# Kernel tuning notes

Measured on AMD Instinct MI355X. Metric: run time of the kernel, lower is better.

Reference implementation:

```python
import jax, jax.numpy as jnp
import numpy as np

B, S, D, H = 2, 2048, 4096, 32
HD = D // H
FF = 22016 // 2  # QWenMLP gets intermediate_size // 2 = 11008
EPS = 1e-6
THETA = 10000.0


def setup_inputs() -> dict:
    key = jax.random.key(0)
    ks = jax.random.split(key, 10)
    s = lambda fan_in: 1.0 / np.sqrt(fan_in)
    return {
        "positions": jnp.broadcast_to(jnp.arange(S, dtype=jnp.int32), (B, S)),
        "hidden_states": jax.random.normal(ks[0], (B, S, D), jnp.float32),
        "ln1_w": jnp.ones((D,), jnp.float32),
        "ln2_w": jnp.ones((D,), jnp.float32),
        "Wqkv": jax.random.normal(ks[1], (D, 3 * D), jnp.float32) * s(D),
        "bqkv": jax.random.normal(ks[2], (3 * D,), jnp.float32) * 0.02,
        "Wo": jax.random.normal(ks[3], (D, D), jnp.float32) * s(D),
        "W1": jax.random.normal(ks[4], (D, FF), jnp.float32) * s(D),
        "W2": jax.random.normal(ks[5], (D, FF), jnp.float32) * s(D),
        "Wout": jax.random.normal(ks[6], (FF, D), jnp.float32) * s(FF),
    }


def _rmsnorm(x, w, eps=EPS):
    return x * jax.lax.rsqrt(jnp.mean(x * x, axis=-1, keepdims=True) + eps) * w


def _rope(x, positions):
    # x: [B, S, H, HD]; NeoX-style rotate-half RoPE over full head_dim
    inv_freq = 1.0 / (THETA ** (jnp.arange(0, HD, 2, dtype=jnp.float32) / HD))
    freqs = positions.astype(jnp.float32)[..., None] * inv_freq  # [B, S, HD/2]
    cos = jnp.concatenate([jnp.cos(freqs)] * 2, axis=-1)[:, :, None, :]
    sin = jnp.concatenate([jnp.sin(freqs)] * 2, axis=-1)[:, :, None, :]
    x1, x2 = jnp.split(x, 2, axis=-1)
    rotated = jnp.concatenate([-x2, x1], axis=-1)
    return x * cos + rotated * sin


def reference(positions, hidden_states, ln1_w, ln2_w, Wqkv, bqkv, Wo, W1, W2, Wout):
    residual = hidden_states
    h = _rmsnorm(hidden_states, ln1_w)
    qkv = h @ Wqkv + bqkv                              # [B, S, 3D]
    q, k, v = jnp.split(qkv, 3, axis=-1)
    q = _rope(q.reshape(B, S, H, HD), positions)
    k = _rope(k.reshape(B, S, H, HD), positions)
    v = v.reshape(B, S, H, HD)
    scores = jnp.einsum("bqhd,bkhd->bhqk", q, k) * (HD ** -0.5)
    causal = jnp.tril(jnp.ones((S, S), bool))
    scores = jnp.where(causal, scores, jnp.finfo(scores.dtype).min)
    probs = jax.nn.softmax(scores, axis=-1)
    attn = jnp.einsum("bhqk,bkhd->bqhd", probs, v).reshape(B, S, D)
    h = residual + attn @ Wo
    residual = h
    h = _rmsnorm(h, ln2_w)
    h = (h @ W1) * jax.nn.silu(h @ W2)                  # SwiGLU: w1(x) * silu(w2(x))
    return residual + h @ Wout
```

## Files before the change

### kernel.cpp

```cpp
#include <hip/hip_runtime.h>

typedef unsigned short u16;
typedef unsigned int   u32;
typedef __bf16 bf16x8 __attribute__((ext_vector_type(8)));
typedef float  f32x4  __attribute__((ext_vector_type(4)));
typedef unsigned short u16x2 __attribute__((ext_vector_type(2)));
typedef unsigned short u16x4 __attribute__((ext_vector_type(4)));
typedef unsigned short u16x8 __attribute__((ext_vector_type(8)));
typedef unsigned int   u32x4 __attribute__((ext_vector_type(4)));

#define DEV __device__ __forceinline__

DEV u16 f2b(float f) {
  u32 u = __builtin_bit_cast(u32, f);
  return (u16)((u + 0x7fffu + ((u >> 16) & 1u)) >> 16);
}
DEV float b2f(u16 h) { u32 u = ((u32)h) << 16; return __builtin_bit_cast(float, u); }

DEV void gload16(const void* g, void* l) {
  __builtin_amdgcn_global_load_lds((__attribute__((address_space(1))) void*)(g),
                                   (__attribute__((address_space(3))) void*)(l),
                                   16, 0, 0);
}

DEV f32x4 MFMA(bf16x8 a, bf16x8 b, f32x4 c) {
  return __builtin_amdgcn_mfma_f32_16x16x32_bf16(a, b, c, 0, 0, 0);
}

DEV u32 ldsoff(const void* p) {
  return (u32)(uintptr_t)(__attribute__((address_space(3))) void*)p;
}
DEV bf16x8 dsr128(u32 a) {
  u32x4 d;
  asm volatile("ds_read_b128 %0, %1" : "=v"(d) : "v"(a) : "memory");
  return __builtin_bit_cast(bf16x8, d);
}

__global__ __launch_bounds__(256) void transpose_cvt(const float* __restrict__ W,
                                                     u16* __restrict__ Wt,
                                                     int K, int N) {
  __shared__ float tile[64][65];
  const int n0 = blockIdx.x * 64, k0 = blockIdx.y * 64;
  const int tx = threadIdx.x, ty = threadIdx.y;
#pragma unroll
  for (int i = 0; i < 16; ++i) {
    const int row = ty + i * 4;
    tile[row][tx] = W[(size_t)(k0 + row) * N + n0 + tx];
  }
  __syncthreads();
#pragma unroll
  for (int i = 0; i < 8; ++i) {
    const int nrow = ty * 2 + (tx >> 5) + i * 8;
    const int kp = (tx & 31) * 2;
    u16x2 v;
    v[0] = f2b(tile[kp][nrow]);
    v[1] = f2b(tile[kp + 1][nrow]);
    *(u16x2*)&Wt[(size_t)(n0 + nrow) * K + k0 + kp] = v;
  }
}

__global__ __launch_bounds__(256) void rmsnorm_k(const float* __restrict__ x,
                                                 const float* __restrict__ w,
                                                 u16* __restrict__ o, int D) {
  const int row = blockIdx.x, tid = threadIdx.x;
  const float4* xr = (const float4*)(x + (size_t)row * D);
  const float4* wr = (const float4*)w;
  float4 v[4];
  float ss = 0.f;
#pragma unroll
  for (int i = 0; i < 4; ++i) {
    v[i] = xr[i * 256 + tid];
    ss += v[i].x * v[i].x + v[i].y * v[i].y + v[i].z * v[i].z + v[i].w * v[i].w;
  }
#pragma unroll
  for (int off = 1; off < 64; off <<= 1) ss += __shfl_xor(ss, off, 64);
  __shared__ float red[4];
  if ((tid & 63) == 0) red[tid >> 6] = ss;
  __syncthreads();
  const float tot = red[0] + red[1] + red[2] + red[3];
  const float sc = rsqrtf(tot / (float)D + 1e-6f);
  u16x4* orow = (u16x4*)(o + (size_t)row * D);
#pragma unroll
  for (int i = 0; i < 4; ++i) {
    float4 wv = wr[i * 256 + tid];
    u16x4 p;
    p[0] = f2b(v[i].x * sc * wv.x);
    p[1] = f2b(v[i].y * sc * wv.y);
    p[2] = f2b(v[i].z * sc * wv.z);
    p[3] = f2b(v[i].w * sc * wv.w);
    orow[i * 256 + tid] = p;
  }
}

__global__ __launch_bounds__(256) void rope_table(const int* __restrict__ positions,
                                                  float* __restrict__ tab, int BS) {
  const int idx = blockIdx.x * 256 + threadIdx.x;
  if (idx >= BS * 64) return;
  const int bs = idx >> 6, i = idx & 63;
  const float pos = (float)positions[bs];
  const float inv = __expf(-(float)i * (9.210340371976184f / 64.f));
  const float ang = pos * inv;
  float s, c;
  sincosf(ang, &s, &c);
  tab[idx] = c;
  tab[BS * 64 + idx] = s;
}

__global__ __launch_bounds__(256) void rope_apply(u16* __restrict__ qkv,
                                                  const float* __restrict__ tab, int BS) {
  const int idx = blockIdx.x * 256 + threadIdx.x;
  if (idx >= BS * 1024) return;
  const int ip = (idx & 31) * 2, h = (idx >> 5) & 31, bs = idx >> 10;
  const float2 c2 = ((const float2*)tab)[bs * 32 + (ip >> 1)];
  const float2 s2 = ((const float2*)(tab + (size_t)BS * 64))[bs * 32 + (ip >> 1)];
  const size_t base = (size_t)bs * 12288 + h * 128 + ip;
  u16x2 a1 = *(const u16x2*)&qkv[base];
  u16x2 a2 = *(const u16x2*)&qkv[base + 64];
  u16x2 b1 = *(const u16x2*)&qkv[base + 4096];
  u16x2 b2 = *(const u16x2*)&qkv[base + 4096 + 64];
  u16x2 r;
  r[0] = f2b(b2f(a1[0]) * c2.x - b2f(a2[0]) * s2.x);
  r[1] = f2b(b2f(a1[1]) * c2.y - b2f(a2[1]) * s2.y);
  *(u16x2*)&qkv[base] = r;
  r[0] = f2b(b2f(a2[0]) * c2.x + b2f(a1[0]) * s2.x);
  r[1] = f2b(b2f(a2[1]) * c2.y + b2f(a1[1]) * s2.y);
  *(u16x2*)&qkv[base + 64] = r;
  r[0] = f2b(b2f(b1[0]) * c2.x - b2f(b2[0]) * s2.x);
  r[1] = f2b(b2f(b1[1]) * c2.y - b2f(b2[1]) * s2.y);
  *(u16x2*)&qkv[base + 4096] = r;
  r[0] = f2b(b2f(b2[0]) * c2.x + b2f(b1[0]) * s2.x);
  r[1] = f2b(b2f(b2[1]) * c2.y + b2f(b1[1]) * s2.y);
  *(u16x2*)&qkv[base + 4096 + 64] = r;
}

template <int MODE>
__global__ __launch_bounds__(512, 2) void gemm256(const u16* __restrict__ A,
                                                  const u16* __restrict__ Bt,
                                                  void* __restrict__ outp,
                                                  const float* __restrict__ bias,
                                                  const float* __restrict__ resid,
                                                  const u16* __restrict__ g1,
                                                  int M, int N, int K) {
  __shared__ __align__(16) u16 As[3 * 8192];
  __shared__ __align__(16) u16 Bs[3 * 8192];
  const int tid = threadIdx.x;
  const int wid = tid >> 6, l = tid & 63;
  const int wm = wid >> 2, wn = wid & 3;
  const int lr = l & 15, lc = l >> 4;
  const int gx = gridDim.x;
  const int nwg = gx * gridDim.y;
  const int orig = blockIdx.y * gx + blockIdx.x;
  const int wg = (orig & 7) * (nwg >> 3) + (orig >> 3);
  const int m0 = (wg / gx) * 256, n0 = (wg % gx) * 256;

  const int NT = K >> 5;
  const int NI = NT >> 1;

  const int rt = tid >> 2;
  const int ct = (tid & 3) ^ ((rt >> 1) & 3);
  const u16* aS = A + (size_t)(m0 + rt) * K + ct * 8;
  const u16* bS = Bt + (size_t)(n0 + rt) * K + ct * 8;

  auto STG = [&](u16* slot, const u16* src, int tk) {
    gload16(src + tk * 32, slot + wid * 512);
    gload16(src + (size_t)128 * K + tk * 32, slot + 4096 + wid * 512);
  };

  const u32 aBase = ldsoff(As), bBase = ldsoff(Bs);
  auto offA = [&](int slot, int mf) {
    const int r = wm * 128 + mf * 16 + lr;
    return aBase + (u32)slot * 16384u + (u32)(r * 64 + ((lc ^ ((r >> 1) & 3)) * 16));
  };
  auto offB = [&](int slot, int nf) {
    const int r = wn * 64 + nf * 16 + lr;
    return bBase + (u32)slot * 16384u + (u32)(r * 64 + ((lc ^ ((r >> 1) & 3)) * 16));
  };

  f32x4 acc[8][4] = {};

#define BAR()  asm volatile("s_barrier" ::: "memory")
#define VM4()  asm volatile("s_waitcnt vmcnt(4)" ::: "memory")
#define VM0()  asm volatile("s_waitcnt vmcnt(0)" ::: "memory")
#define LGKM0_FENCE() do { asm volatile("s_waitcnt lgkmcnt(0)" ::: "memory"); \
                           __builtin_amdgcn_sched_barrier(0); } while (0)

  STG(&As[0], aS, 0);
  STG(&Bs[0], bS, 0);
  STG(&As[8192], aS, 1);
  STG(&Bs[8192], bS, 1);
  VM4();
  BAR();

  int sa = 0, sb = 1, sc = 2;
  for (int i = 0; i < NI; ++i) {
    const int Tc = 2 * i + 2, Td = 2 * i + 3;
    u16* Aa = &As[sa * 8192]; u16* Ba = &Bs[sa * 8192];
    u16* Ac = &As[sc * 8192]; u16* Bc = &Bs[sc * 8192];
    bf16x8 af[8], b0, b1;
#pragma unroll
    for (int mf = 0; mf < 8; ++mf) af[mf] = dsr128(offA(sa, mf));
    b0 = dsr128(offB(sa, 0)); b1 = dsr128(offB(sa, 1));
    if (Tc < NT) STG(Ac, aS, Tc);
    BAR();
    LGKM0_FENCE();
    __builtin_amdgcn_s_setprio(1);
#pragma unroll
    for (int mf = 0; mf < 8; ++mf) {
      acc[mf][0] = MFMA(af[mf], b0, acc[mf][0]);
      acc[mf][1] = MFMA(af[mf], b1, acc[mf][1]);
    }
    __builtin_amdgcn_s_setprio(0);
    BAR();
    b0 = dsr128(offB(sa, 2)); b1 = dsr128(offB(sa, 3));
    if (Tc < NT) STG(Bc, bS, Tc);
    BAR();
    LGKM0_FENCE();
    __builtin_amdgcn_s_setprio(1);
#pragma unroll
    for (int mf = 0; mf < 8; ++mf) {
      acc[mf][2] = MFMA(af[mf], b0, acc[mf][2]);
      acc[mf][3] = MFMA(af[mf], b1, acc[mf][3]);
    }
    __builtin_amdgcn_s_setprio(0);
    if (Tc < NT) VM4(); else VM0();
    BAR();
#pragma unroll
    for (int mf = 0; mf < 8; ++mf) af[mf] = dsr128(offA(sb, mf));
    b0 = dsr128(offB(sb, 0)); b1 = dsr128(offB(sb, 1));
    if (Td < NT) STG(Aa, aS, Td);
    BAR();
    LGKM0_FENCE();
    __builtin_amdgcn_s_setprio(1);
#pragma unroll
    for (int mf = 0; mf < 8; ++mf) {
      acc[mf][0] = MFMA(af[mf], b0, acc[mf][0]);
      acc[mf][1] = MFMA(af[mf], b1, acc[mf][1]);
    }
    __builtin_amdgcn_s_setprio(0);
    BAR();
    b0 = dsr128(offB(sb, 2)); b1 = dsr128(offB(sb, 3));
    if (Td < NT) STG(Ba, bS, Td);
    BAR();
    LGKM0_FENCE();
    __builtin_amdgcn_s_setprio(1);
#pragma unroll
    for (int mf = 0; mf < 8; ++mf) {
      acc[mf][2] = MFMA(af[mf], b0, acc[mf][2]);
      acc[mf][3] = MFMA(af[mf], b1, acc[mf][3]);
    }
    __builtin_amdgcn_s_setprio(0);
    if (Td < NT) VM4(); else VM0();
    BAR();
    const int t = sc; sc = sb; sb = sa; sa = t;
  }
#undef BAR
#undef VM4
#undef VM0
#undef LGKM0_FENCE

#pragma unroll
  for (int mf = 0; mf < 8; ++mf) {
#pragma unroll
    for (int nf = 0; nf < 4; ++nf) {
      const int gr = m0 + wm * 128 + mf * 16 + lc * 4;
      const int gc = n0 + wn * 64 + nf * 16 + lr;
#pragma unroll
      for (int r = 0; r < 4; ++r) {
        float v = acc[mf][nf][r];
        const size_t idx = (size_t)(gr + r) * N + gc;
        if constexpr (MODE == 0) {
          ((u16*)outp)[idx] = f2b(v);
        } else if constexpr (MODE == 1) {
          ((u16*)outp)[idx] = f2b(v + bias[gc]);
        } else if constexpr (MODE == 2) {
          ((float*)outp)[idx] = v + resid[idx];
        } else {
          const float g = b2f(g1[idx]);
          const float sv = v / (1.f + __expf(-v));
          ((u16*)outp)[idx] = f2b(g * sv);
        }
      }
    }
  }
}

__global__ __launch_bounds__(256) void attn_kernel(const u16* __restrict__ qkv,
                                                   u16* __restrict__ o, int S) {
  const int qtile = gridDim.x - 1 - blockIdx.x;
  const int bh = blockIdx.y;
  const int b = bh >> 5, h = bh & 31;
  const int q0 = qtile * 64;
  const int tid = threadIdx.x;
  const int w = tid >> 6, l = tid & 63;
  const int lr = l & 15, lc = l >> 4;
  const size_t RS = 12288;
  const float SCALE = 0.08838834764831845f;

  __shared__ __align__(16) u16 Ks[64 * 128];
  __shared__ __align__(16) u16 Vt[128 * 64];
  __shared__ __align__(16) u16 Ps[4][16 * 64];

  bf16x8 qf[4];
  {
    const u16* qp = qkv + (size_t)(b * S + q0 + w * 16 + lr) * RS + h * 128 + 8 * lc;
#pragma unroll
    for (int kc = 0; kc < 4; ++kc) qf[kc] = *(const bf16x8*)(qp + kc * 32);
  }

  float m_[4], ls[4];
  f32x4 O[8] = {};
#pragma unroll
  for (int r = 0; r < 4; ++r) { m_[r] = -3e38f; ls[r] = 0.f; }

  const int nkt = qtile + 1;
  for (int kt = 0; kt < nkt; ++kt) {
    const int k0 = kt * 64;
#pragma unroll
    for (int it = 0; it < 4; ++it) {
      const int eid = it * 256 + tid;
      const int kr = eid >> 4, d0 = (eid & 15) * 8;
      u16x8 k8 = *(const u16x8*)(qkv + (size_t)(b * S + k0 + kr) * RS + 4096 + h * 128 + d0);
      *(u16x8*)&Ks[kr * 128 + (d0 ^ ((kr & 7) * 8))] = k8;
    }
#pragma unroll
    for (int it = 0; it < 4; ++it) {
      const int d0 = (it * 4 + w) * 8;
      u16x8 v8 = *(const u16x8*)(qkv + (size_t)(b * S + k0 + l) * RS + 8192 + h * 128 + d0);
#pragma unroll
      for (int jj = 0; jj < 8; ++jj) {
        const int d = d0 + jj;
        Vt[(d * 64 + l) ^ ((d & 7) * 8)] = v8[jj];
      }
    }
    __syncthreads();

    const int nks = (kt == qtile) ? (w + 1) : 4;
    float sv[4][4];
#pragma unroll
    for (int ks = 0; ks < 4; ++ks) {
      if (ks < nks) {
        const int row = ks * 16 + lr;
        f32x4 sacc = {0.f, 0.f, 0.f, 0.f};
#pragma unroll
        for (int kc = 0; kc < 4; ++kc) {
          bf16x8 kf = *(const bf16x8*)&Ks[row * 128 + ((kc * 32 + 8 * lc) ^ ((lr & 7) * 8))];
          sacc = MFMA(qf[kc], kf, sacc);
        }
        const bool dm = (kt == qtile) && (ks == w);
#pragma unroll
        for (int r = 0; r < 4; ++r) {
          float x = sacc[r] * SCALE;
          if (dm) {
            const int kg = ks * 16 + lr, qg = w * 16 + lc * 4 + r;
            if (kg > qg) x = -3e38f;
          }
          sv[ks][r] = x;
        }
      } else {
#pragma unroll
        for (int r = 0; r < 4; ++r) sv[ks][r] = -3e38f;
      }
    }

    float alpha[4];
#pragma unroll
    for (int r = 0; r < 4; ++r) {
      float pm = fmaxf(fmaxf(sv[0][r], sv[1][r]), fmaxf(sv[2][r], sv[3][r]));
#pragma unroll
      for (int off = 1; off < 16; off <<= 1) pm = fmaxf(pm, __shfl_xor(pm, off, 64));
      const float mn = fmaxf(m_[r], pm);
      alpha[r] = __expf(m_[r] - mn);
      m_[r] = mn;
    }
    float p[4][4];
#pragma unroll
    for (int ks = 0; ks < 4; ++ks)
#pragma unroll
      for (int r = 0; r < 4; ++r) {
        p[ks][r] = __expf(sv[ks][r] - m_[r]);
        const int q = lc * 4 + r, k = ks * 16 + lr;
        Ps[w][q * 64 + (k ^ ((q & 7) * 8))] = f2b(p[ks][r]);
      }
#pragma unroll
    for (int r = 0; r < 4; ++r) {
      float s = p[0][r] + p[1][r] + p[2][r] + p[3][r];
#pragma unroll
      for (int off = 1; off < 16; off <<= 1) s += __shfl_xor(s, off, 64);
      ls[r] = ls[r] * alpha[r] + s;
    }
#pragma unroll
    for (int dt = 0; dt < 8; ++dt)
#pragma unroll
      for (int r = 0; r < 4; ++r) O[dt][r] *= alpha[r];

#pragma unroll
    for (int half = 0; half < 2; ++half) {
      const bf16x8 ap = *(const bf16x8*)&Ps[w][lr * 64 + ((half * 32 + 8 * lc) ^ ((lr & 7) * 8))];
#pragma unroll
      for (int dt = 0; dt < 8; ++dt) {
        const int d = dt * 16 + lr;
        const bf16x8 bv = *(const bf16x8*)&Vt[d * 64 + ((half * 32 + 8 * lc) ^ ((d & 7) * 8))];
        O[dt] = MFMA(ap, bv, O[dt]);
      }
    }
    __syncthreads();
  }

  float inv[4];
#pragma unroll
  for (int r = 0; r < 4; ++r) inv[r] = 1.f / ls[r];
#pragma unroll
  for (int dt = 0; dt < 8; ++dt)
#pragma unroll
    for (int r = 0; r < 4; ++r) {
      const int qg = q0 + w * 16 + lc * 4 + r;
      o[(size_t)(b * S + qg) * 4096 + h * 128 + dt * 16 + lr] = f2b(O[dt][r] * inv[r]);
    }
}

extern "C" void kernel_launch(void* const* d_in, const int* in_sizes, int n_in,
                              void* d_out, int out_size, void* d_ws, size_t ws_size,
                              hipStream_t stream) {
  const int*   positions = (const int*)d_in[0];
  const float* hidden    = (const float*)d_in[1];
  const float* ln1       = (const float*)d_in[2];
  const float* ln2       = (const float*)d_in[3];
  const float* Wqkv      = (const float*)d_in[4];
  const float* bqkv      = (const float*)d_in[5];
  const float* Wo        = (const float*)d_in[6];
  const float* W1        = (const float*)d_in[7];
  const float* W2        = (const float*)d_in[8];
  const float* Wout      = (const float*)d_in[9];
  float* out = (float*)d_out;

  const int S = 2048, BS = 4096, D = 4096, FF = 11008, N3 = 12288;

  char* ws = (char*)d_ws;
  size_t off = 0;
  auto alloc = [&](size_t bytes) { void* p = ws + off; off += (bytes + 255) & ~(size_t)255; return p; };
  u16*   WT    = (u16*)alloc((size_t)N3 * D * 2);
  u16*   qkv   = (u16*)alloc((size_t)BS * N3 * 2);
  u16*   slotH = (u16*)alloc((size_t)BS * D * 2);
  float* h2    = (float*)alloc((size_t)BS * D * 4);
  u16*   slotG = (u16*)alloc((size_t)BS * FF * 2);
  float* tab   = (float*)alloc((size_t)2 * BS * 64 * 4);
  if (ws_size < off) return;

  rope_table<<<(BS * 64 + 255) / 256, 256, 0, stream>>>(positions, tab, BS);

  transpose_cvt<<<dim3(N3 / 64, D / 64), dim3(64, 4), 0, stream>>>(Wqkv, WT, D, N3);
  rmsnorm_k<<<BS, 256, 0, stream>>>(hidden, ln1, slotH, D);
  gemm256<1><<<dim3(N3 / 256, BS / 256), 512, 0, stream>>>(slotH, WT, qkv, bqkv, nullptr, nullptr, BS, N3, D);
  rope_apply<<<(BS * 1024) / 256, 256, 0, stream>>>(qkv, tab, BS);

  attn_kernel<<<dim3(S / 64, 64), 256, 0, stream>>>(qkv, slotH, S);

  transpose_cvt<<<dim3(D / 64, D / 64), dim3(64, 4), 0, stream>>>(Wo, WT, D, D);
  gemm256<2><<<dim3(D / 256, BS / 256), 512, 0, stream>>>(slotH, WT, h2, nullptr, hidden, nullptr, BS, D, D);

  rmsnorm_k<<<BS, 256, 0, stream>>>(h2, ln2, slotH, D);
  transpose_cvt<<<dim3(FF / 64, D / 64), dim3(64, 4), 0, stream>>>(W1, WT, D, FF);
  gemm256<0><<<dim3(FF / 256, BS / 256), 512, 0, stream>>>(slotH, WT, slotG, nullptr, nullptr, nullptr, BS, FF, D);
  transpose_cvt<<<dim3(FF / 64, D / 64), dim3(64, 4), 0, stream>>>(W2, WT, D, FF);
  gemm256<3><<<dim3(FF / 256, BS / 256), 512, 0, stream>>>(slotH, WT, slotG, nullptr, nullptr, slotG, BS, FF, D);
  transpose_cvt<<<dim3(D / 64, FF / 64), dim3(64, 4), 0, stream>>>(Wout, WT, FF, D);
  gemm256<2><<<dim3(D / 256, BS / 256), 512, 0, stream>>>(slotG, WT, out, nullptr, h2, nullptr, BS, D, FF);
}
```

Before: 2.286 ms.

## Fuse W1 and W2 GEMMs into one SwiGLU GEMM kernel

```diff
diff --git a/kernel.cpp b/kernel.cpp
--- a/kernel.cpp
+++ b/kernel.cpp
@@ -139,7 +139,6 @@
                                                   void* __restrict__ outp,
                                                   const float* __restrict__ bias,
                                                   const float* __restrict__ resid,
-                                                  const u16* __restrict__ g1,
                                                   int M, int N, int K) {
   __shared__ __align__(16) u16 As[3 * 8192];
   __shared__ __align__(16) u16 Bs[3 * 8192];
@@ -272,13 +271,153 @@
           ((u16*)outp)[idx] = f2b(v);
         } else if constexpr (MODE == 1) {
           ((u16*)outp)[idx] = f2b(v + bias[gc]);
-        } else if constexpr (MODE == 2) {
+        } else {
           ((float*)outp)[idx] = v + resid[idx];
-        } else {
-          const float g = b2f(g1[idx]);
-          const float sv = v / (1.f + __expf(-v));
-          ((u16*)outp)[idx] = f2b(g * sv);
         }
+      }
+    }
+  }
+}
+
+__global__ __launch_bounds__(512, 2) void gemm_swiglu(const u16* __restrict__ A,
+                                                      const u16* __restrict__ W1t,
+                                                      const u16* __restrict__ W2t,
+                                                      u16* __restrict__ outp,
+                                                      int M, int N, int K) {
+  __shared__ __align__(16) u16 As[3 * 8192];
+  __shared__ __align__(16) u16 Bs[3 * 8192];
+  const int tid = threadIdx.x;
+  const int wid = tid >> 6, l = tid & 63;
+  const int wm = wid >> 2, wn = wid & 3;
+  const int lr = l & 15, lc = l >> 4;
+  const int gx = gridDim.x;
+  const int nwg = gx * gridDim.y;
+  const int orig = blockIdx.y * gx + blockIdx.x;
+  const int wg = (orig & 7) * (nwg >> 3) + (orig >> 3);
+  const int m0 = (wg / gx) * 256, n0 = (wg % gx) * 128;
+
+  const int NT = K >> 5;
+  const int NI = NT >> 1;
+
+  const int rt = tid >> 2;
+  const int ct = (tid & 3) ^ ((rt >> 1) & 3);
+  const u16* aS  = A   + (size_t)(m0 + rt) * K + ct * 8;
+  const u16* b1S = W1t + (size_t)(n0 + rt) * K + ct * 8;
+  const u16* b2S = W2t + (size_t)(n0 + rt) * K + ct * 8;
+
+  auto STGA = [&](u16* slot, int tk) {
+    gload16(aS + tk * 32, slot + wid * 512);
+    gload16(aS + (size_t)128 * K + tk * 32, slot + 4096 + wid * 512);
+  };
+  auto STGB = [&](u16* slot, int tk) {
+    gload16(b1S + tk * 32, slot + wid * 512);
+    gload16(b2S + tk * 32, slot + 4096 + wid * 512);
+  };
+
+  const u32 aBase = ldsoff(As), bBase = ldsoff(Bs);
+  auto offA = [&](int slot, int mf) {
+    const int r = wm * 128 + mf * 16 + lr;
+    return aBase + (u32)slot * 16384u + (u32)(r * 64 + ((lc ^ ((r >> 1) & 3)) * 16));
+  };
+  auto offB = [&](int slot, int nf) {
+    const int r = (nf < 2) ? (wn * 32 + nf * 16 + lr) : (128 + wn * 32 + (nf - 2) * 16 + lr);
+    return bBase + (u32)slot * 16384u + (u32)(r * 64 + ((lc ^ ((r >> 1) & 3)) * 16));
+  };
+
+  f32x4 acc[8][4] = {};
+
+#define BAR()  asm volatile("s_barrier" ::: "memory")
+#define VM4()  asm volatile("s_waitcnt vmcnt(4)" ::: "memory")
+#define VM0()  asm volatile("s_waitcnt vmcnt(0)" ::: "memory")
+#define LGKM0_FENCE() do { asm volatile("s_waitcnt lgkmcnt(0)" ::: "memory"); \
+                           __builtin_amdgcn_sched_barrier(0); } while (0)
+
+  STGA(&As[0], 0);
+  STGB(&Bs[0], 0);
+  STGA(&As[8192], 1);
+  STGB(&Bs[8192], 1);
+  VM4();
+  BAR();
+
+  int sa = 0, sb = 1, sc = 2;
+  for (int i = 0; i < NI; ++i) {
+    const int Tc = 2 * i + 2, Td = 2 * i + 3;
+    u16* Aa = &As[sa * 8192]; u16* Ba = &Bs[sa * 8192];
+    u16* Ac = &As[sc * 8192]; u16* Bc = &Bs[sc * 8192];
+    bf16x8 af[8], b0, b1;
+#pragma unroll
+    for (int mf = 0; mf < 8; ++mf) af[mf] = dsr128(offA(sa, mf));
+    b0 = dsr128(offB(sa, 0)); b1 = dsr128(offB(sa, 1));
+    if (Tc < NT) STGA(Ac, Tc);
+    BAR();
+    LGKM0_FENCE();
+    __builtin_amdgcn_s_setprio(1);
+#pragma unroll
+    for (int mf = 0; mf < 8; ++mf) {
+      acc[mf][0] = MFMA(af[mf], b0, acc[mf][0]);
+      acc[mf][1] = MFMA(af[mf], b1, acc[mf][1]);
+    }
+    __builtin_amdgcn_s_setprio(0);
+    BAR();
+    b0 = dsr128(offB(sa, 2)); b1 = dsr128(offB(sa, 3));
+    if (Tc < NT) STGB(Bc, Tc);
+    BAR();
+    LGKM0_FENCE();
+    __builtin_amdgcn_s_setprio(1);
+#pragma unroll
+    for (int mf = 0; mf < 8; ++mf) {
+      acc[mf][2] = MFMA(af[mf], b0, acc[mf][2]);
+      acc[mf][3] = MFMA(af[mf], b1, acc[mf][3]);
+    }
+    __builtin_amdgcn_s_setprio(0);
+    if (Tc < NT) VM4(); else VM0();
+    BAR();
+#pragma unroll
+    for (int mf = 0; mf < 8; ++mf) af[mf] = dsr128(offA(sb, mf));
+    b0 = dsr128(offB(sb, 0)); b1 = dsr128(offB(sb, 1));
+    if (Td < NT) STGA(Aa, Td);
+    BAR();
+    LGKM0_FENCE();
+    __builtin_amdgcn_s_setprio(1);
+#pragma unroll
+    for (int mf = 0; mf < 8; ++mf) {
+      acc[mf][0] = MFMA(af[mf], b0, acc[mf][0]);
+      acc[mf][1] = MFMA(af[mf], b1, acc[mf][1]);
+    }
+    __builtin_amdgcn_s_setprio(0);
+    BAR();
+    b0 = dsr128(offB(sb, 2)); b1 = dsr128(offB(sb, 3));
+    if (Td < NT) STGB(Ba, Td);
+    BAR();
+    LGKM0_FENCE();
+    __builtin_amdgcn_s_setprio(1);
+#pragma unroll
+    for (int mf = 0; mf < 8; ++mf) {
+      acc[mf][2] = MFMA(af[mf], b0, acc[mf][2]);
+      acc[mf][3] = MFMA(af[mf], b1, acc[mf][3]);
+    }
+    __builtin_amdgcn_s_setprio(0);
+    if (Td < NT) VM4(); else VM0();
+    BAR();
+    const int t = sc; sc = sb; sb = sa; sa = t;
+  }
+#undef BAR
+#undef VM4
+#undef VM0
+#undef LGKM0_FENCE
+
+#pragma unroll
+  for (int mf = 0; mf < 8; ++mf) {
+#pragma unroll
+    for (int nf = 0; nf < 2; ++nf) {
+      const int gr = m0 + wm * 128 + mf * 16 + lc * 4;
+      const int gc = n0 + wn * 32 + nf * 16 + lr;
+#pragma unroll
+      for (int r = 0; r < 4; ++r) {
+        const float g1 = acc[mf][nf][r];
+        const float g2 = acc[mf][nf + 2][r];
+        const float sv = g2 / (1.f + __expf(-g2));
+        outp[(size_t)(gr + r) * N + gc] = f2b(g1 * sv);
       }
     }
   }
@@ -450,19 +589,18 @@
 
   transpose_cvt<<<dim3(N3 / 64, D / 64), dim3(64, 4), 0, stream>>>(Wqkv, WT, D, N3);
   rmsnorm_k<<<BS, 256, 0, stream>>>(hidden, ln1, slotH, D);
-  gemm256<1><<<dim3(N3 / 256, BS / 256), 512, 0, stream>>>(slotH, WT, qkv, bqkv, nullptr, nullptr, BS, N3, D);
+  gemm256<1><<<dim3(N3 / 256, BS / 256), 512, 0, stream>>>(slotH, WT, qkv, bqkv, nullptr, BS, N3, D);
   rope_apply<<<(BS * 1024) / 256, 256, 0, stream>>>(qkv, tab, BS);
 
   attn_kernel<<<dim3(S / 64, 64), 256, 0, stream>>>(qkv, slotH, S);
 
   transpose_cvt<<<dim3(D / 64, D / 64), dim3(64, 4), 0, stream>>>(Wo, WT, D, D);
-  gemm256<2><<<dim3(D / 256, BS / 256), 512, 0, stream>>>(slotH, WT, h2, nullptr, hidden, nullptr, BS, D, D);
+  gemm256<2><<<dim3(D / 256, BS / 256), 512, 0, stream>>>(slotH, WT, h2, nullptr, hidden, BS, D, D);
 
   rmsnorm_k<<<BS, 256, 0, stream>>>(h2, ln2, slotH, D);
   transpose_cvt<<<dim3(FF / 64, D / 64), dim3(64, 4), 0, stream>>>(W1, WT, D, FF);
-  gemm256<0><<<dim3(FF / 256, BS / 256), 512, 0, stream>>>(slotH, WT, slotG, nullptr, nullptr, nullptr, BS, FF, D);
-  transpose_cvt<<<dim3(FF / 64, D / 64), dim3(64, 4), 0, stream>>>(W2, WT, D, FF);
-  gemm256<3><<<dim3(FF / 256, BS / 256), 512, 0, stream>>>(slotH, WT, slotG, nullptr, nullptr, slotG, BS, FF, D);
+  transpose_cvt<<<dim3(FF / 64, D / 64), dim3(64, 4), 0, stream>>>(W2, qkv, D, FF);
+  gemm_swiglu<<<dim3(FF / 128, BS / 256), 512, 0, stream>>>(slotH, WT, qkv, slotG, BS, FF, D);
   transpose_cvt<<<dim3(D / 64, FF / 64), dim3(64, 4), 0, stream>>>(Wout, WT, FF, D);
-  gemm256<2><<<dim3(D / 256, BS / 256), 512, 0, stream>>>(slotG, WT, out, nullptr, h2, nullptr, BS, D, FF);
-}
+  gemm256<2><<<dim3(D / 256, BS / 256), 512, 0, stream>>>(slotG, WT, out, nullptr, h2, BS, D, FF);
+}
```

Measured after the change: 2.243 ms. About the same (-1.9%).
